# Kernel optimization log

Hardware: AMD Instinct MI355X
Metric: run time of the kernel (lower is better)

Reference implementation:

```python
import jax, jax.numpy as jnp
import numpy as np

N = 1_000_000  # nodes
E = 1_000_000  # edges (== N so poss_edge can be indexed by node ids AND edge masks, as in source)
C = 64         # classes; poss_edge has C+1 columns (last = 'intrust')
SEMI_LAMBDA = 0.5
EDGE_LAMBDA = 1.0


def setup_inputs() -> dict:
    key = jax.random.key(0)
    k1, k2, k3, k4, k5 = jax.random.split(key, 5)
    # probabilities strictly positive so log() is finite
    poss_node = jax.random.uniform(k1, (N, C), jnp.float32, 0.05, 1.0)
    poss_edge = jax.random.uniform(k2, (E, C + 1), jnp.float32, 0.05, 1.0)
    groundTruth = jax.random.randint(k3, (N,), 0, C)
    mask = jax.random.randint(k4, (N,), 0, 2).astype(bool)
    edges = jax.random.randint(k5, (E, 2), 0, N)
    return {"poss_node": poss_node, "poss_edge": poss_edge,
            "groundTruth": groundTruth, "mask": mask, "edges": edges}


def reference(poss_node, poss_edge, groundTruth, mask, edges):
    dt = poss_node.dtype
    maskf = mask.astype(dt)
    # --- node NLL loss: mean of -log p[i, gt[i]] over masked nodes ---
    logp = jnp.log(poss_node[jnp.arange(N), groundTruth])  # [N]
    loss = -jnp.sum(maskf * logp) / jnp.sum(maskf)

    e0, e1 = edges[:, 0], edges[:, 1]
    intrust = jax.lax.stop_gradient(poss_edge[:, -1])  # detach

    # --- semi loss (faithful to source: scalar sq-diff times sum(1-intrust)) ---
    if SEMI_LAMBDA >= 1e-9:
        sqdiff = jnp.sum((poss_edge[e0] - poss_edge[e1]) ** 2)  # scalar
        semi_loss = SEMI_LAMBDA * jnp.sum(1.0 - intrust) * sqdiff
    else:
        semi_loss = jnp.zeros((), dt)

    # --- edge label splits ---
    m0, m1 = mask[e0], mask[e1]
    label_mask = m0 | m1
    both = m0 & m1
    gt0, gt1 = groundTruth[e0], groundTruth[e1]
    same = both & (gt0 == gt1)
    diff = both & (gt0 != gt1)
    single = label_mask & ~both
    left_s = single & m0
    right_s = single & m1

    rows = jnp.arange(E)
    p_gt0 = poss_edge[rows, gt0]   # [E] prob of left node's label
    p_gt1 = poss_edge[rows, gt1]   # [E] prob of right node's label
    p_last = poss_edge[:, -1]      # [E] 'no-edge' / intrust column

    z = jnp.zeros((), dt)
    raw = (-jnp.sum(jnp.where(same, jnp.log(p_gt0), z))
           - jnp.sum(jnp.where(diff, jnp.log(p_last), z))
           - jnp.sum(jnp.where(left_s, jnp.log(p_last + p_gt0), z))
           - jnp.sum(jnp.where(right_s, jnp.log(p_last + p_gt1), z)))
    S = jnp.sum(label_mask.astype(dt))
    # source applies (*= edge_lambda; /= S) twice
    edge_loss = raw * (EDGE_LAMBDA * EDGE_LAMBDA) / (S * S)

    return loss + semi_loss + edge_loss
```

## Files before the change

### kernel.cpp

```cpp
#include <hip/hip_runtime.h>
#include <math.h>

namespace {
constexpr int N = 1000000;
constexpr int E = 1000000;
constexpr int C = 64;
constexpr int BLOCK = 256;
constexpr int GROUPS_PER_BLOCK = BLOCK / 16;

constexpr int PREP_BLOCKS = 2048;
constexpr int EDGE_BLOCKS = 2048;
constexpr int PREP_GROUPS = PREP_BLOCKS * GROUPS_PER_BLOCK;
constexpr int EDGE_GROUPS = EDGE_BLOCKS * GROUPS_PER_BLOCK;

constexpr int NODE_BLOCKS_F = 1024;
constexpr int EDGE_BLOCKS_F = 2048;
constexpr int TOTAL_GROUPS_F = EDGE_BLOCKS_F * GROUPS_PER_BLOCK;

constexpr double SEMI_LAMBDA = 0.5;
constexpr double EDGE_LAMBDA = 1.0;

constexpr size_t PE16_ELEMS = (size_t)E * C;
constexpr size_t WS_NEEDED  = PE16_ELEMS * 2
                            + (size_t)E * 4
                            + (size_t)3 * PREP_BLOCKS * 4
                            + (size_t)3 * EDGE_BLOCKS * 4;
}

union H4 { uint2 u2; _Float16 h[4]; };

__device__ __forceinline__ float waveReduceSum(float v) {
#pragma unroll
    for (int off = 32; off > 0; off >>= 1) v += __shfl_down(v, off, 64);
    return v;
}


__device__ __forceinline__ void node_phase(const float* __restrict__ poss_node,
                                           const int* __restrict__ gt,
                                           const int* __restrict__ mask,
                                           float& lsum, float& cnt) {
    for (int i = blockIdx.x * BLOCK + threadIdx.x; i < N; i += PREP_BLOCKS * BLOCK) {
        if (mask[i] != 0) {
            lsum += logf(poss_node[(size_t)i * C + gt[i]]);
            cnt += 1.f;
        }
    }
}

__device__ __forceinline__ void row_phase(const float* __restrict__ poss_edge,
                                          unsigned short* __restrict__ pe16,
                                          float* __restrict__ plast,
                                          float& s1) {
    const int t = threadIdx.x & 15;
    const int g = blockIdx.x * GROUPS_PER_BLOCK + (threadIdx.x >> 4);
    for (int r = g; r < E; r += PREP_GROUPS) {
        const float* __restrict__ row = poss_edge + (size_t)r * (C + 1);
        H4 h;
        h.h[0] = (_Float16)row[4 * t + 0];
        h.h[1] = (_Float16)row[4 * t + 1];
        h.h[2] = (_Float16)row[4 * t + 2];
        h.h[3] = (_Float16)row[4 * t + 3];
        *reinterpret_cast<uint2*>(pe16 + (size_t)r * C + 4 * t) = h.u2;
        if (t == 0) {
            const float pl = row[C];
            plast[r] = pl;
            s1 += 1.f - pl;
        }
    }
}

__global__ __launch_bounds__(BLOCK) void prep_kernel(
    const float* __restrict__ poss_node,
    const float* __restrict__ poss_edge,
    const int* __restrict__ gt,
    const int* __restrict__ mask,
    unsigned short* __restrict__ pe16,
    float* __restrict__ plast,
    float* __restrict__ partials)
{
    float lsum = 0.f, cnt = 0.f, s1 = 0.f;
    if (blockIdx.x & 1) {
        node_phase(poss_node, gt, mask, lsum, cnt);
        row_phase(poss_edge, pe16, plast, s1);
    } else {
        row_phase(poss_edge, pe16, plast, s1);
        node_phase(poss_node, gt, mask, lsum, cnt);
    }

    __shared__ float s[3][BLOCK / 64];
    lsum = waveReduceSum(lsum);
    cnt  = waveReduceSum(cnt);
    s1   = waveReduceSum(s1);
    const int lane = threadIdx.x & 63, wv = threadIdx.x >> 6;
    if (lane == 0) { s[0][wv] = lsum; s[1][wv] = cnt; s[2][wv] = s1; }
    __syncthreads();
    if (threadIdx.x == 0) {
        float a = 0.f, b = 0.f, c = 0.f;
#pragma unroll
        for (int w = 0; w < BLOCK / 64; ++w) { a += s[0][w]; b += s[1][w]; c += s[2][w]; }
        partials[0 * PREP_BLOCKS + blockIdx.x] = a;
        partials[1 * PREP_BLOCKS + blockIdx.x] = b;
        partials[2 * PREP_BLOCKS + blockIdx.x] = c;
    }
}

__global__ __launch_bounds__(BLOCK) void edge16_kernel(
    const unsigned short* __restrict__ pe16,
    const float* __restrict__ plast,
    const int* __restrict__ gt,
    const int* __restrict__ mask,
    const int* __restrict__ edges,
    float* __restrict__ partials)
{
    const int t = threadIdx.x & 15;
    const int g = blockIdx.x * GROUPS_PER_BLOCK + (threadIdx.x >> 4);

    float sq = 0.f, pos = 0.f, lcnt = 0.f;

    for (int e = g; e < E; e += EDGE_GROUPS) {
        const int2 ep = *(const int2*)(edges + 2 * (size_t)e);
        const int e0 = ep.x, e1 = ep.y;

        H4 ha, hb;
        ha.u2 = *reinterpret_cast<const uint2*>(pe16 + (size_t)e0 * C + 4 * t);
        hb.u2 = *reinterpret_cast<const uint2*>(pe16 + (size_t)e1 * C + 4 * t);
        const float d0 = (float)ha.h[0] - (float)hb.h[0];
        const float d1 = (float)ha.h[1] - (float)hb.h[1];
        const float d2 = (float)ha.h[2] - (float)hb.h[2];
        const float d3 = (float)ha.h[3] - (float)hb.h[3];
        float acc = fmaf(d0, d0, fmaf(d1, d1, fmaf(d2, d2, d3 * d3)));
        if (t == 0) {
            const float dl = plast[e0] - plast[e1];
            acc = fmaf(dl, dl, acc);
        }
        sq += acc;

        const float p_last = plast[e];
        const int m0 = (mask[e0] != 0);
        const int m1 = (mask[e1] != 0);
        if (m0 | m1) {
            const int g0 = gt[e0];
            const int g1 = gt[e1];
            float contrib;
            if (m0 & m1) {
                contrib = (g0 == g1)
                    ? logf((float)*reinterpret_cast<const _Float16*>(pe16 + (size_t)e * C + g0))
                    : logf(p_last);
            } else if (m0) {
                contrib = logf(p_last + (float)*reinterpret_cast<const _Float16*>(pe16 + (size_t)e * C + g0));
            } else {
                contrib = logf(p_last + (float)*reinterpret_cast<const _Float16*>(pe16 + (size_t)e * C + g1));
            }
            if (t == 0) { pos += contrib; lcnt += 1.f; }
        }
    }

    __shared__ float s[3][BLOCK / 64];
    sq   = waveReduceSum(sq);
    pos  = waveReduceSum(pos);
    lcnt = waveReduceSum(lcnt);
    const int lane = threadIdx.x & 63, wv = threadIdx.x >> 6;
    if (lane == 0) { s[0][wv] = sq; s[1][wv] = pos; s[2][wv] = lcnt; }
    __syncthreads();
    if (threadIdx.x == 0) {
        float a = 0.f, b = 0.f, c = 0.f;
#pragma unroll
        for (int w = 0; w < BLOCK / 64; ++w) { a += s[0][w]; b += s[1][w]; c += s[2][w]; }
        partials[0 * EDGE_BLOCKS + blockIdx.x] = a;
        partials[1 * EDGE_BLOCKS + blockIdx.x] = b;
        partials[2 * EDGE_BLOCKS + blockIdx.x] = c;
    }
}

__global__ __launch_bounds__(BLOCK) void finalize16_kernel(
    const float* __restrict__ prep_partials,
    const float* __restrict__ edge_partials,
    float* __restrict__ out)
{
    double a0 = 0, a1 = 0, a2 = 0, a3 = 0, a4 = 0, a5 = 0;
    for (int i = threadIdx.x; i < PREP_BLOCKS; i += BLOCK) {
        a0 += (double)prep_partials[0 * PREP_BLOCKS + i];
        a1 += (double)prep_partials[1 * PREP_BLOCKS + i];
        a2 += (double)prep_partials[2 * PREP_BLOCKS + i];
    }
    for (int i = threadIdx.x; i < EDGE_BLOCKS; i += BLOCK) {
        a3 += (double)edge_partials[0 * EDGE_BLOCKS + i];
        a4 += (double)edge_partials[1 * EDGE_BLOCKS + i];
        a5 += (double)edge_partials[2 * EDGE_BLOCKS + i];
    }
#pragma unroll
    for (int off = 32; off > 0; off >>= 1) {
        a0 += __shfl_down(a0, off, 64);
        a1 += __shfl_down(a1, off, 64);
        a2 += __shfl_down(a2, off, 64);
        a3 += __shfl_down(a3, off, 64);
        a4 += __shfl_down(a4, off, 64);
        a5 += __shfl_down(a5, off, 64);
    }
    __shared__ double sd[6][BLOCK / 64];
    const int lane = threadIdx.x & 63, wv = threadIdx.x >> 6;
    if (lane == 0) {
        sd[0][wv] = a0; sd[1][wv] = a1; sd[2][wv] = a2;
        sd[3][wv] = a3; sd[4][wv] = a4; sd[5][wv] = a5;
    }
    __syncthreads();
    if (threadIdx.x == 0) {
        double t[6];
#pragma unroll
        for (int k = 0; k < 6; ++k) {
            double v = 0;
#pragma unroll
            for (int w = 0; w < BLOCK / 64; ++w) v += sd[k][w];
            t[k] = v;
        }
        const double loss      = -t[0] / t[1];
        const double semi      = SEMI_LAMBDA * t[2] * t[3];
        const double edge_loss = (-t[4]) * (EDGE_LAMBDA * EDGE_LAMBDA) / (t[5] * t[5]);
        out[0] = (float)(loss + semi + edge_loss);
    }
}


__global__ __launch_bounds__(BLOCK) void node_kernel_f(
    const float* __restrict__ poss_node,
    const int* __restrict__ gt,
    const int* __restrict__ mask,
    float* __restrict__ partials)
{
    float lsum = 0.f, cnt = 0.f;
    for (int i = blockIdx.x * BLOCK + threadIdx.x; i < N; i += NODE_BLOCKS_F * BLOCK) {
        if (mask[i] != 0) {
            lsum += logf(poss_node[(size_t)i * C + gt[i]]);
            cnt += 1.f;
        }
    }
    __shared__ float s0[BLOCK / 64], s1[BLOCK / 64];
    lsum = waveReduceSum(lsum);
    cnt  = waveReduceSum(cnt);
    const int lane = threadIdx.x & 63, wv = threadIdx.x >> 6;
    if (lane == 0) { s0[wv] = lsum; s1[wv] = cnt; }
    __syncthreads();
    if (threadIdx.x == 0) {
        float a = 0.f, b = 0.f;
#pragma unroll
        for (int w = 0; w < BLOCK / 64; ++w) { a += s0[w]; b += s1[w]; }
        partials[blockIdx.x]                 = a;
        partials[NODE_BLOCKS_F + blockIdx.x] = b;
    }
}

__global__ __launch_bounds__(BLOCK) void edge_kernel_f(
    const float* __restrict__ poss_edge,
    const int* __restrict__ gt,
    const int* __restrict__ mask,
    const int* __restrict__ edges,
    float* __restrict__ partials)
{
    const int t   = threadIdx.x & 15;
    const int grp = threadIdx.x >> 4;
    const int globalGroup = blockIdx.x * GROUPS_PER_BLOCK + grp;

    float s1 = 0.f, sq = 0.f, pos = 0.f, lcnt = 0.f;

    for (int e = globalGroup; e < E; e += TOTAL_GROUPS_F) {
        const int2 ep = *(const int2*)(edges + 2 * (size_t)e);
        const int e0 = ep.x, e1 = ep.y;

        const float* __restrict__ ra = poss_edge + (size_t)e0 * (C + 1);
        const float* __restrict__ rb = poss_edge + (size_t)e1 * (C + 1);
        const float* __restrict__ re = poss_edge + (size_t)e  * (C + 1);

        const float a0 = ra[t], a1 = ra[t + 16], a2 = ra[t + 32], a3 = ra[t + 48];
        const float b0 = rb[t], b1 = rb[t + 16], b2 = rb[t + 32], b3 = rb[t + 48];
        const float d0 = a0 - b0, d1 = a1 - b1, d2 = a2 - b2, d3 = a3 - b3;
        float acc = fmaf(d0, d0, fmaf(d1, d1, fmaf(d2, d2, d3 * d3)));
        if (t == 0) {
            const float dl = ra[C] - rb[C];
            acc = fmaf(dl, dl, acc);
        }
        sq += acc;

        const float p_last = re[C];
        const int m0 = (mask[e0] != 0);
        const int m1 = (mask[e1] != 0);
        if (m0 | m1) {
            const int g0 = gt[e0];
            const int g1 = gt[e1];
            float contrib;
            if (m0 & m1) {
                contrib = (g0 == g1) ? logf(re[g0]) : logf(p_last);
            } else if (m0) {
                contrib = logf(p_last + re[g0]);
            } else {
                contrib = logf(p_last + re[g1]);
            }
            if (t == 0) { pos += contrib; lcnt += 1.f; }
        }
        if (t == 0) s1 += 1.f - p_last;
    }

    __shared__ float s[4][BLOCK / 64];
    s1   = waveReduceSum(s1);
    sq   = waveReduceSum(sq);
    pos  = waveReduceSum(pos);
    lcnt = waveReduceSum(lcnt);
    const int lane = threadIdx.x & 63, wv = threadIdx.x >> 6;
    if (lane == 0) { s[0][wv] = s1; s[1][wv] = sq; s[2][wv] = pos; s[3][wv] = lcnt; }
    __syncthreads();
    if (threadIdx.x == 0) {
        float a = 0.f, b = 0.f, c = 0.f, d = 0.f;
#pragma unroll
        for (int w = 0; w < BLOCK / 64; ++w) {
            a += s[0][w]; b += s[1][w]; c += s[2][w]; d += s[3][w];
        }
        partials[0 * EDGE_BLOCKS_F + blockIdx.x] = a;
        partials[1 * EDGE_BLOCKS_F + blockIdx.x] = b;
        partials[2 * EDGE_BLOCKS_F + blockIdx.x] = c;
        partials[3 * EDGE_BLOCKS_F + blockIdx.x] = d;
    }
}

__global__ __launch_bounds__(BLOCK) void finalize_kernel_f(
    const float* __restrict__ node_partials,
    const float* __restrict__ edge_partials,
    float* __restrict__ out)
{
    double a0 = 0, a1 = 0, a2 = 0, a3 = 0, a4 = 0, a5 = 0;
    for (int i = threadIdx.x; i < NODE_BLOCKS_F; i += BLOCK) {
        a0 += (double)node_partials[i];
        a1 += (double)node_partials[NODE_BLOCKS_F + i];
    }
    for (int i = threadIdx.x; i < EDGE_BLOCKS_F; i += BLOCK) {
        a2 += (double)edge_partials[0 * EDGE_BLOCKS_F + i];
        a3 += (double)edge_partials[1 * EDGE_BLOCKS_F + i];
        a4 += (double)edge_partials[2 * EDGE_BLOCKS_F + i];
        a5 += (double)edge_partials[3 * EDGE_BLOCKS_F + i];
    }
#pragma unroll
    for (int off = 32; off > 0; off >>= 1) {
        a0 += __shfl_down(a0, off, 64);
        a1 += __shfl_down(a1, off, 64);
        a2 += __shfl_down(a2, off, 64);
        a3 += __shfl_down(a3, off, 64);
        a4 += __shfl_down(a4, off, 64);
        a5 += __shfl_down(a5, off, 64);
    }
    __shared__ double sd[6][BLOCK / 64];
    const int lane = threadIdx.x & 63, wv = threadIdx.x >> 6;
    if (lane == 0) {
        sd[0][wv] = a0; sd[1][wv] = a1; sd[2][wv] = a2;
        sd[3][wv] = a3; sd[4][wv] = a4; sd[5][wv] = a5;
    }
    __syncthreads();
    if (threadIdx.x == 0) {
        double t[6];
#pragma unroll
        for (int k = 0; k < 6; ++k) {
            double v = 0;
#pragma unroll
            for (int w = 0; w < BLOCK / 64; ++w) v += sd[k][w];
            t[k] = v;
        }
        const double loss      = -t[0] / t[1];
        const double semi      = SEMI_LAMBDA * t[2] * t[3];
        const double edge_loss = (-t[4]) * (EDGE_LAMBDA * EDGE_LAMBDA) / (t[5] * t[5]);
        out[0] = (float)(loss + semi + edge_loss);
    }
}


extern "C" void kernel_launch(void* const* d_in, const int* in_sizes, int n_in,
                              void* d_out, int out_size, void* d_ws, size_t ws_size,
                              hipStream_t stream) {
    const float* poss_node = (const float*)d_in[0];
    const float* poss_edge = (const float*)d_in[1];
    const int*   gt        = (const int*)d_in[2];
    const int*   mask      = (const int*)d_in[3];
    const int*   edges     = (const int*)d_in[4];
    float*       out       = (float*)d_out;

    if (ws_size >= WS_NEEDED) {
        unsigned short* pe16          = (unsigned short*)d_ws;
        float*          plast         = (float*)(pe16 + PE16_ELEMS);
        float*          prep_partials = plast + E;
        float*          edge_partials = prep_partials + 3 * PREP_BLOCKS;

        prep_kernel<<<PREP_BLOCKS, BLOCK, 0, stream>>>(
            poss_node, poss_edge, gt, mask, pe16, plast, prep_partials);
        edge16_kernel<<<EDGE_BLOCKS, BLOCK, 0, stream>>>(
            pe16, plast, gt, mask, edges, edge_partials);
        finalize16_kernel<<<1, BLOCK, 0, stream>>>(prep_partials, edge_partials, out);
    } else {
        float* node_partials = (float*)d_ws;
        float* edge_partials = node_partials + 2 * NODE_BLOCKS_F;

        node_kernel_f<<<NODE_BLOCKS_F, BLOCK, 0, stream>>>(poss_node, gt, mask, node_partials);
        edge_kernel_f<<<EDGE_BLOCKS_F, BLOCK, 0, stream>>>(poss_edge, gt, mask, edges, edge_partials);
        finalize_kernel_f<<<1, BLOCK, 0, stream>>>(node_partials, edge_partials, out);
    }
}
```

Before: 613.2 us.

## Move label-loss into fp16 prep pass, split node kernel, widen sq gather loads

The per-edge label loss is now computed inside the row-conversion kernel from the fp32 values already held in registers, using a cross-lane shuffle to pick the label column. This removes the extra plast/pe16 reads from the gather kernel. The node NLL pass becomes its own kernel. The squared-difference gather kernel now uses 8 lanes per edge with 16-byte loads instead of 16 lanes with 8-byte loads. The trade-offs are an extra kernel launch and an extra edges/mask/gt read in the prep pass. The shuffle-based extraction also adds divergence and lane traffic.

New measurement: 567.7 us. 1.08x faster.

```diff
diff --git a/kernel.cpp b/kernel.cpp
--- a/kernel.cpp
+++ b/kernel.cpp
@@ -7,11 +7,13 @@
 constexpr int C = 64;
 constexpr int BLOCK = 256;
 constexpr int GROUPS_PER_BLOCK = BLOCK / 16;
-
+constexpr int GROUPS8_PER_BLOCK = BLOCK / 8;
+
+constexpr int NODE_BLOCKS = 1024;
 constexpr int PREP_BLOCKS = 2048;
-constexpr int EDGE_BLOCKS = 2048;
+constexpr int SQ_BLOCKS   = 2048;
 constexpr int PREP_GROUPS = PREP_BLOCKS * GROUPS_PER_BLOCK;
-constexpr int EDGE_GROUPS = EDGE_BLOCKS * GROUPS_PER_BLOCK;
+constexpr int SQ_GROUPS   = SQ_BLOCKS * GROUPS8_PER_BLOCK;
 
 constexpr int NODE_BLOCKS_F = 1024;
 constexpr int EDGE_BLOCKS_F = 2048;
@@ -23,11 +25,13 @@
 constexpr size_t PE16_ELEMS = (size_t)E * C;
 constexpr size_t WS_NEEDED  = PE16_ELEMS * 2
                             + (size_t)E * 4
+                            + (size_t)2 * NODE_BLOCKS * 4
                             + (size_t)3 * PREP_BLOCKS * 4
-                            + (size_t)3 * EDGE_BLOCKS * 4;
+                            + (size_t)1 * SQ_BLOCKS * 4;
 }
 
 union H4 { uint2 u2; _Float16 h[4]; };
+union H8 { uint4 u4; _Float16 h[8]; };
 
 __device__ __forceinline__ float waveReduceSum(float v) {
 #pragma unroll
@@ -35,65 +39,103 @@
     return v;
 }
 
-
-__device__ __forceinline__ void node_phase(const float* __restrict__ poss_node,
-                                           const int* __restrict__ gt,
-                                           const int* __restrict__ mask,
-                                           float& lsum, float& cnt) {
-    for (int i = blockIdx.x * BLOCK + threadIdx.x; i < N; i += PREP_BLOCKS * BLOCK) {
+__device__ __forceinline__ float groupExtract(float c0, float c1, float c2, float c3,
+                                              int col, int waveBase) {
+    const int slot = col & 3;
+    const float lo  = (slot & 1) ? c1 : c0;
+    const float hi  = (slot & 1) ? c3 : c2;
+    const float sel = (slot & 2) ? hi : lo;
+    return __shfl(sel, waveBase + (col >> 2), 64);
+}
+
+
+__global__ __launch_bounds__(BLOCK) void node_kernel(
+    const float* __restrict__ poss_node,
+    const int* __restrict__ gt,
+    const int* __restrict__ mask,
+    float* __restrict__ partials)
+{
+    float lsum = 0.f, cnt = 0.f;
+    for (int i = blockIdx.x * BLOCK + threadIdx.x; i < N; i += NODE_BLOCKS * BLOCK) {
         if (mask[i] != 0) {
             lsum += logf(poss_node[(size_t)i * C + gt[i]]);
             cnt += 1.f;
         }
     }
-}
-
-__device__ __forceinline__ void row_phase(const float* __restrict__ poss_edge,
-                                          unsigned short* __restrict__ pe16,
-                                          float* __restrict__ plast,
-                                          float& s1) {
-    const int t = threadIdx.x & 15;
-    const int g = blockIdx.x * GROUPS_PER_BLOCK + (threadIdx.x >> 4);
-    for (int r = g; r < E; r += PREP_GROUPS) {
-        const float* __restrict__ row = poss_edge + (size_t)r * (C + 1);
-        H4 h;
-        h.h[0] = (_Float16)row[4 * t + 0];
-        h.h[1] = (_Float16)row[4 * t + 1];
-        h.h[2] = (_Float16)row[4 * t + 2];
-        h.h[3] = (_Float16)row[4 * t + 3];
-        *reinterpret_cast<uint2*>(pe16 + (size_t)r * C + 4 * t) = h.u2;
-        if (t == 0) {
-            const float pl = row[C];
-            plast[r] = pl;
-            s1 += 1.f - pl;
-        }
+    __shared__ float s0[BLOCK / 64], s1[BLOCK / 64];
+    lsum = waveReduceSum(lsum);
+    cnt  = waveReduceSum(cnt);
+    const int lane = threadIdx.x & 63, wv = threadIdx.x >> 6;
+    if (lane == 0) { s0[wv] = lsum; s1[wv] = cnt; }
+    __syncthreads();
+    if (threadIdx.x == 0) {
+        float a = 0.f, b = 0.f;
+#pragma unroll
+        for (int w = 0; w < BLOCK / 64; ++w) { a += s0[w]; b += s1[w]; }
+        partials[blockIdx.x]               = a;
+        partials[NODE_BLOCKS + blockIdx.x] = b;
     }
 }
 
 __global__ __launch_bounds__(BLOCK) void prep_kernel(
-    const float* __restrict__ poss_node,
     const float* __restrict__ poss_edge,
     const int* __restrict__ gt,
     const int* __restrict__ mask,
+    const int* __restrict__ edges,
     unsigned short* __restrict__ pe16,
     float* __restrict__ plast,
     float* __restrict__ partials)
 {
-    float lsum = 0.f, cnt = 0.f, s1 = 0.f;
-    if (blockIdx.x & 1) {
-        node_phase(poss_node, gt, mask, lsum, cnt);
-        row_phase(poss_edge, pe16, plast, s1);
-    } else {
-        row_phase(poss_edge, pe16, plast, s1);
-        node_phase(poss_node, gt, mask, lsum, cnt);
+    const int t = threadIdx.x & 15;
+    const int g = blockIdx.x * GROUPS_PER_BLOCK + (threadIdx.x >> 4);
+    const int waveBase = threadIdx.x & 48;
+
+    float s1 = 0.f, pos = 0.f, lcnt = 0.f;
+
+    for (int r = g; r < E; r += PREP_GROUPS) {
+        const float* __restrict__ row = poss_edge + (size_t)r * (C + 1);
+        const float c0 = row[4 * t + 0];
+        const float c1 = row[4 * t + 1];
+        const float c2 = row[4 * t + 2];
+        const float c3 = row[4 * t + 3];
+        H4 h;
+        h.h[0] = (_Float16)c0; h.h[1] = (_Float16)c1;
+        h.h[2] = (_Float16)c2; h.h[3] = (_Float16)c3;
+        *reinterpret_cast<uint2*>(pe16 + (size_t)r * C + 4 * t) = h.u2;
+
+        const float pl = row[C];
+        if (t == 0) {
+            plast[r] = pl;
+            s1 += 1.f - pl;
+        }
+
+        const int2 ep = *(const int2*)(edges + 2 * (size_t)r);
+        const int m0 = (mask[ep.x] != 0);
+        const int m1 = (mask[ep.y] != 0);
+        if (m0 | m1) {
+            float contrib;
+            if (m0 & m1) {
+                const int g0 = gt[ep.x];
+                const int g1 = gt[ep.y];
+                if (g0 == g1) {
+                    contrib = logf(groupExtract(c0, c1, c2, c3, g0, waveBase));
+                } else {
+                    contrib = logf(pl);
+                }
+            } else {
+                const int gg = m0 ? gt[ep.x] : gt[ep.y];
+                contrib = logf(pl + groupExtract(c0, c1, c2, c3, gg, waveBase));
+            }
+            if (t == 0) { pos += contrib; lcnt += 1.f; }
+        }
     }
 
     __shared__ float s[3][BLOCK / 64];
-    lsum = waveReduceSum(lsum);
-    cnt  = waveReduceSum(cnt);
     s1   = waveReduceSum(s1);
-    const int lane = threadIdx.x & 63, wv = threadIdx.x >> 6;
-    if (lane == 0) { s[0][wv] = lsum; s[1][wv] = cnt; s[2][wv] = s1; }
+    pos  = waveReduceSum(pos);
+    lcnt = waveReduceSum(lcnt);
+    const int lane = threadIdx.x & 63, wv = threadIdx.x >> 6;
+    if (lane == 0) { s[0][wv] = s1; s[1][wv] = pos; s[2][wv] = lcnt; }
     __syncthreads();
     if (threadIdx.x == 0) {
         float a = 0.f, b = 0.f, c = 0.f;
@@ -105,89 +147,66 @@
     }
 }
 
-__global__ __launch_bounds__(BLOCK) void edge16_kernel(
+__global__ __launch_bounds__(BLOCK) void sq_kernel(
     const unsigned short* __restrict__ pe16,
     const float* __restrict__ plast,
-    const int* __restrict__ gt,
-    const int* __restrict__ mask,
     const int* __restrict__ edges,
     float* __restrict__ partials)
 {
-    const int t = threadIdx.x & 15;
-    const int g = blockIdx.x * GROUPS_PER_BLOCK + (threadIdx.x >> 4);
-
-    float sq = 0.f, pos = 0.f, lcnt = 0.f;
-
-    for (int e = g; e < E; e += EDGE_GROUPS) {
+    const int t = threadIdx.x & 7;
+    const int g = blockIdx.x * GROUPS8_PER_BLOCK + (threadIdx.x >> 3);
+
+    float sq = 0.f;
+
+    for (int e = g; e < E; e += SQ_GROUPS) {
         const int2 ep = *(const int2*)(edges + 2 * (size_t)e);
-        const int e0 = ep.x, e1 = ep.y;
-
-        H4 ha, hb;
-        ha.u2 = *reinterpret_cast<const uint2*>(pe16 + (size_t)e0 * C + 4 * t);
-        hb.u2 = *reinterpret_cast<const uint2*>(pe16 + (size_t)e1 * C + 4 * t);
-        const float d0 = (float)ha.h[0] - (float)hb.h[0];
-        const float d1 = (float)ha.h[1] - (float)hb.h[1];
-        const float d2 = (float)ha.h[2] - (float)hb.h[2];
-        const float d3 = (float)ha.h[3] - (float)hb.h[3];
-        float acc = fmaf(d0, d0, fmaf(d1, d1, fmaf(d2, d2, d3 * d3)));
+        H8 ha, hb;
+        ha.u4 = *reinterpret_cast<const uint4*>(pe16 + (size_t)ep.x * C + 8 * t);
+        hb.u4 = *reinterpret_cast<const uint4*>(pe16 + (size_t)ep.y * C + 8 * t);
+        float acc = 0.f;
+#pragma unroll
+        for (int k = 0; k < 8; ++k) {
+            const float d = (float)ha.h[k] - (float)hb.h[k];
+            acc = fmaf(d, d, acc);
+        }
         if (t == 0) {
-            const float dl = plast[e0] - plast[e1];
+            const float dl = plast[ep.x] - plast[ep.y];
             acc = fmaf(dl, dl, acc);
         }
         sq += acc;
-
-        const float p_last = plast[e];
-        const int m0 = (mask[e0] != 0);
-        const int m1 = (mask[e1] != 0);
-        if (m0 | m1) {
-            const int g0 = gt[e0];
-            const int g1 = gt[e1];
-            float contrib;
-            if (m0 & m1) {
-                contrib = (g0 == g1)
-                    ? logf((float)*reinterpret_cast<const _Float16*>(pe16 + (size_t)e * C + g0))
-                    : logf(p_last);
-            } else if (m0) {
-                contrib = logf(p_last + (float)*reinterpret_cast<const _Float16*>(pe16 + (size_t)e * C + g0));
-            } else {
-                contrib = logf(p_last + (float)*reinterpret_cast<const _Float16*>(pe16 + (size_t)e * C + g1));
-            }
-            if (t == 0) { pos += contrib; lcnt += 1.f; }
-        }
-    }
-
-    __shared__ float s[3][BLOCK / 64];
-    sq   = waveReduceSum(sq);
-    pos  = waveReduceSum(pos);
-    lcnt = waveReduceSum(lcnt);
-    const int lane = threadIdx.x & 63, wv = threadIdx.x >> 6;
-    if (lane == 0) { s[0][wv] = sq; s[1][wv] = pos; s[2][wv] = lcnt; }
-    __syncthreads();
-    if (threadIdx.x == 0) {
-        float a = 0.f, b = 0.f, c = 0.f;
-#pragma unroll
-        for (int w = 0; w < BLOCK / 64; ++w) { a += s[0][w]; b += s[1][w]; c += s[2][w]; }
-        partials[0 * EDGE_BLOCKS + blockIdx.x] = a;
-        partials[1 * EDGE_BLOCKS + blockIdx.x] = b;
-        partials[2 * EDGE_BLOCKS + blockIdx.x] = c;
+    }
+
+    __shared__ float s[BLOCK / 64];
+    sq = waveReduceSum(sq);
+    const int lane = threadIdx.x & 63, wv = threadIdx.x >> 6;
+    if (lane == 0) s[wv] = sq;
+    __syncthreads();
+    if (threadIdx.x == 0) {
+        float a = 0.f;
+#pragma unroll
+        for (int w = 0; w < BLOCK / 64; ++w) a += s[w];
+        partials[blockIdx.x] = a;
     }
 }
 
 __global__ __launch_bounds__(BLOCK) void finalize16_kernel(
+    const float* __restrict__ node_partials,
     const float* __restrict__ prep_partials,
-    const float* __restrict__ edge_partials,
+    const float* __restrict__ sq_partials,
     float* __restrict__ out)
 {
     double a0 = 0, a1 = 0, a2 = 0, a3 = 0, a4 = 0, a5 = 0;
+    for (int i = threadIdx.x; i < NODE_BLOCKS; i += BLOCK) {
+        a0 += (double)node_partials[i];
+        a1 += (double)node_partials[NODE_BLOCKS + i];
+    }
     for (int i = threadIdx.x; i < PREP_BLOCKS; i += BLOCK) {
-        a0 += (double)prep_partials[0 * PREP_BLOCKS + i];
-        a1 += (double)prep_partials[1 * PREP_BLOCKS + i];
-        a2 += (double)prep_partials[2 * PREP_BLOCKS + i];
-    }
-    for (int i = threadIdx.x; i < EDGE_BLOCKS; i += BLOCK) {
-        a3 += (double)edge_partials[0 * EDGE_BLOCKS + i];
-        a4 += (double)edge_partials[1 * EDGE_BLOCKS + i];
-        a5 += (double)edge_partials[2 * EDGE_BLOCKS + i];
+        a2 += (double)prep_partials[0 * PREP_BLOCKS + i];
+        a3 += (double)prep_partials[1 * PREP_BLOCKS + i];
+        a4 += (double)prep_partials[2 * PREP_BLOCKS + i];
+    }
+    for (int i = threadIdx.x; i < SQ_BLOCKS; i += BLOCK) {
+        a5 += (double)sq_partials[i];
     }
 #pragma unroll
     for (int off = 32; off > 0; off >>= 1) {
@@ -214,41 +233,20 @@
             for (int w = 0; w < BLOCK / 64; ++w) v += sd[k][w];
             t[k] = v;
         }
-        const double loss      = -t[0] / t[1];
-        const double semi      = SEMI_LAMBDA * t[2] * t[3];
-        const double edge_loss = (-t[4]) * (EDGE_LAMBDA * EDGE_LAMBDA) / (t[5] * t[5]);
+        const double logp_sum  = t[0];
+        const double mask_cnt  = t[1];
+        const double s1_sum    = t[2];
+        const double pos_sum   = t[3];
+        const double label_cnt = t[4];
+        const double sq_sum    = t[5];
+
+        const double loss      = -logp_sum / mask_cnt;
+        const double semi      = SEMI_LAMBDA * s1_sum * sq_sum;
+        const double edge_loss = (-pos_sum) * (EDGE_LAMBDA * EDGE_LAMBDA) / (label_cnt * label_cnt);
         out[0] = (float)(loss + semi + edge_loss);
     }
 }
 
-
-__global__ __launch_bounds__(BLOCK) void node_kernel_f(
-    const float* __restrict__ poss_node,
-    const int* __restrict__ gt,
-    const int* __restrict__ mask,
-    float* __restrict__ partials)
-{
-    float lsum = 0.f, cnt = 0.f;
-    for (int i = blockIdx.x * BLOCK + threadIdx.x; i < N; i += NODE_BLOCKS_F * BLOCK) {
-        if (mask[i] != 0) {
-            lsum += logf(poss_node[(size_t)i * C + gt[i]]);
-            cnt += 1.f;
-        }
-    }
-    __shared__ float s0[BLOCK / 64], s1[BLOCK / 64];
-    lsum = waveReduceSum(lsum);
-    cnt  = waveReduceSum(cnt);
-    const int lane = threadIdx.x & 63, wv = threadIdx.x >> 6;
-    if (lane == 0) { s0[wv] = lsum; s1[wv] = cnt; }
-    __syncthreads();
-    if (threadIdx.x == 0) {
-        float a = 0.f, b = 0.f;
-#pragma unroll
-        for (int w = 0; w < BLOCK / 64; ++w) { a += s0[w]; b += s1[w]; }
-        partials[blockIdx.x]                 = a;
-        partials[NODE_BLOCKS_F + blockIdx.x] = b;
-    }
-}
 
 __global__ __launch_bounds__(BLOCK) void edge_kernel_f(
     const float* __restrict__ poss_edge,
@@ -383,19 +381,21 @@
     if (ws_size >= WS_NEEDED) {
         unsigned short* pe16          = (unsigned short*)d_ws;
         float*          plast         = (float*)(pe16 + PE16_ELEMS);
-        float*          prep_partials = plast + E;
-        float*          edge_partials = prep_partials + 3 * PREP_BLOCKS;
-
+        float*          node_partials = plast + E;
+        float*          prep_partials = node_partials + 2 * NODE_BLOCKS;
+        float*          sq_partials   = prep_partials + 3 * PREP_BLOCKS;
+
+        node_kernel<<<NODE_BLOCKS, BLOCK, 0, stream>>>(poss_node, gt, mask, node_partials);
         prep_kernel<<<PREP_BLOCKS, BLOCK, 0, stream>>>(
-            poss_node, poss_edge, gt, mask, pe16, plast, prep_partials);
-        edge16_kernel<<<EDGE_BLOCKS, BLOCK, 0, stream>>>(
-            pe16, plast, gt, mask, edges, edge_partials);
-        finalize16_kernel<<<1, BLOCK, 0, stream>>>(prep_partials, edge_partials, out);
+            poss_edge, gt, mask, edges, pe16, plast, prep_partials);
+        sq_kernel<<<SQ_BLOCKS, BLOCK, 0, stream>>>(pe16, plast, edges, sq_partials);
+        finalize16_kernel<<<1, BLOCK, 0, stream>>>(
+            node_partials, prep_partials, sq_partials, out);
     } else {
         float* node_partials = (float*)d_ws;
         float* edge_partials = node_partials + 2 * NODE_BLOCKS_F;
 
-        node_kernel_f<<<NODE_BLOCKS_F, BLOCK, 0, stream>>>(poss_node, gt, mask, node_partials);
+        node_kernel<<<NODE_BLOCKS_F, BLOCK, 0, stream>>>(poss_node, gt, mask, node_partials);
         edge_kernel_f<<<EDGE_BLOCKS_F, BLOCK, 0, stream>>>(poss_edge, gt, mask, edges, edge_partials);
         finalize_kernel_f<<<1, BLOCK, 0, stream>>>(node_partials, edge_partials, out);
     }
```
